# Performance work log

Measured on AMD Instinct MI355X. Metric: run time of the kernel, lower is better.

## Reference

```python
import jax, jax.numpy as jnp
import numpy as np

N = 16384
IN_F = 128
OUT_F = 32


def setup_inputs() -> dict:
    key = jax.random.key(0)
    k1, k2, k3 = jax.random.split(key, 3)
    inp = jax.random.normal(k1, (N, IN_F), dtype=jnp.float32)
    # dense (densified-sparse) adjacency, nonnegative like a normalized adj
    adj = jax.random.uniform(k2, (N, N), dtype=jnp.float32) * (1.0 / N)
    stdv = np.sqrt(1.0 / (IN_F + OUT_F)).astype(np.float32)
    weight = jax.random.uniform(k3, (IN_F, OUT_F), dtype=jnp.float32,
                                minval=-stdv, maxval=stdv)
    return {"input": inp, "adj": adj, "weight": weight}


def reference(input, adj, weight):
    # dropout p=0.0 -> identity (matches nn.Dropout(0.0) / eval mode)
    support = input @ weight          # [N, out_features]
    output = adj @ support            # [N, out_features] neighbor aggregation
    return jax.nn.relu(output)
```

## Files before the change

kernel.cpp:

```cpp
#include <hip/hip_runtime.h>

#define N 16384
#define IN_F 128
#define OUT_F 32
#define NSPLIT 8
#define KR (N / NSPLIT)
#define KC 128
#define CHUNKS (KR / KC)
#define ROWS 32

typedef __attribute__((ext_vector_type(8))) short short8v;
typedef __attribute__((ext_vector_type(4))) float float4v;

#define GLOAD_LDS16(g, l) \
    __builtin_amdgcn_global_load_lds((const __attribute__((address_space(1))) void*)(g), \
                                     (__attribute__((address_space(3))) void*)(l), 16, 0, 0)

__device__ __forceinline__ unsigned short f2bf(float x) {
    unsigned int u = __float_as_uint(x);
    u += 0x7FFFu + ((u >> 16) & 1u);
    return (unsigned short)(u >> 16);
}

__global__ __launch_bounds__(256) void gcn_support(const float* __restrict__ inp,
                                                   const float* __restrict__ w,
                                                   unsigned short* __restrict__ supB) {
    __shared__ float wl[IN_F * OUT_F];
    int tid = threadIdx.x;
#pragma unroll
    for (int u = 0; u < 4; ++u) {
        int idx = (u * 256 + tid) * 4;
        *(float4*)&wl[idx] = *(const float4*)&w[idx];
    }
    __syncthreads();

    int gid = blockIdx.x * 256 + tid;
    int i  = gid >> 2;
    int ks = gid & 3;

    float acc[OUT_F];
#pragma unroll
    for (int j = 0; j < OUT_F; ++j) acc[j] = 0.f;

    const float* ip = inp + (size_t)i * IN_F + ks * 32;
#pragma unroll
    for (int kb = 0; kb < 8; ++kb) {
        float4 a4 = *(const float4*)(ip + kb * 4);
        float av[4] = {a4.x, a4.y, a4.z, a4.w};
#pragma unroll
        for (int kk = 0; kk < 4; ++kk) {
            int k = ks * 32 + kb * 4 + kk;
            const float* wr = &wl[k * OUT_F];
#pragma unroll
            for (int j4 = 0; j4 < 8; ++j4) {
                float4 w4 = *(const float4*)(wr + j4 * 4);
                acc[j4 * 4 + 0] = fmaf(av[kk], w4.x, acc[j4 * 4 + 0]);
                acc[j4 * 4 + 1] = fmaf(av[kk], w4.y, acc[j4 * 4 + 1]);
                acc[j4 * 4 + 2] = fmaf(av[kk], w4.z, acc[j4 * 4 + 2]);
                acc[j4 * 4 + 3] = fmaf(av[kk], w4.w, acc[j4 * 4 + 3]);
            }
        }
    }
#pragma unroll
    for (int j = 0; j < OUT_F; ++j) {
        acc[j] += __shfl_xor(acc[j], 1);
        acc[j] += __shfl_xor(acc[j], 2);
    }
#pragma unroll
    for (int jj = 0; jj < 8; ++jj) {
        int j = ks * 8 + jj;
        supB[(size_t)j * N + i] = f2bf(acc[j]);
    }
}

__global__ __launch_bounds__(256, 5) void gcn_aggregate(const float* __restrict__ adj,
                                                        const unsigned short* __restrict__ supB,
                                                        float* __restrict__ out) {
    __shared__ float sA[2][ROWS * KC];

    int wg = blockIdx.x;
    int rb = wg >> 3;
    int sp = wg & 7;
    int tid  = threadIdx.x;
    int wv   = tid >> 6;
    int lane = tid & 63;
    int mt = wv >> 1;
    int nt = wv & 1;
    int lrow = lane & 15;
    int kgrp = lane >> 4;

    int rowblk = rb * ROWS;
    int kbase  = sp * KR;

    float4v acc = {0.f, 0.f, 0.f, 0.f};

    auto stage = [&](int buf, int c) {
#pragma unroll
        for (int u = 0; u < 4; ++u) {
            int f    = u * 256 + tid;
            int row  = f >> 5;
            int gblk = (f & 31) ^ (row & 7);
            const float* gp = adj + (size_t)(rowblk + row) * N + kbase + c * KC + gblk * 4;
            float* lp = &sA[buf][(u * 256 + wv * 64) * 4];
            GLOAD_LDS16(gp, lp);
        }
    };

    int rowA = mt * 16 + lrow;
    int sw   = rowA & 7;
    const unsigned short* bprow = supB + (size_t)(nt * 16 + lrow) * N + kbase + kgrp * 8;

    stage(0, 0);
    __syncthreads();

    for (int c = 0; c < CHUNKS; ++c) {
        int cur = c & 1;
        if (c + 1 < CHUNKS) stage(cur ^ 1, c + 1);

        const unsigned short* bp = bprow + c * KC;
        short8v b0 = *(const short8v*)(bp + 0);
        short8v b1 = *(const short8v*)(bp + 32);
        short8v b2 = *(const short8v*)(bp + 64);
        short8v b3 = *(const short8v*)(bp + 96);

#pragma unroll
        for (int w = 0; w < 4; ++w) {
            int kw   = w * 32;
            int blk0 = rowA * 32 + (kw >> 2) + kgrp * 2;
            float4 a0 = *(const float4*)&sA[cur][((blk0 ^ sw) << 2)];
            float4 a1 = *(const float4*)&sA[cur][(((blk0 + 1) ^ sw) << 2)];
            short8v af;
            af[0] = (short)f2bf(a0.x); af[1] = (short)f2bf(a0.y);
            af[2] = (short)f2bf(a0.z); af[3] = (short)f2bf(a0.w);
            af[4] = (short)f2bf(a1.x); af[5] = (short)f2bf(a1.y);
            af[6] = (short)f2bf(a1.z); af[7] = (short)f2bf(a1.w);
            short8v bf = (w == 0) ? b0 : (w == 1) ? b1 : (w == 2) ? b2 : b3;
            acc = __builtin_amdgcn_mfma_f32_16x16x32_bf16(af, bf, acc, 0, 0, 0);
        }
        __syncthreads();
    }

    int orow = rowblk + mt * 16 + kgrp * 4;
    int ocol = nt * 16 + lrow;
#pragma unroll
    for (int r = 0; r < 4; ++r)
        atomicAdd(&out[(size_t)(orow + r) * OUT_F + ocol], acc[r]);
}

__global__ __launch_bounds__(256) void gcn_relu(float* __restrict__ out) {
    int gid = blockIdx.x * 256 + threadIdx.x;
    float4* p = (float4*)out;
    float4 v = p[gid];
    v.x = fmaxf(v.x, 0.f);
    v.y = fmaxf(v.y, 0.f);
    v.z = fmaxf(v.z, 0.f);
    v.w = fmaxf(v.w, 0.f);
    p[gid] = v;
}

extern "C" void kernel_launch(void* const* d_in, const int* in_sizes, int n_in,
                              void* d_out, int out_size, void* d_ws, size_t ws_size,
                              hipStream_t stream) {
    (void)in_sizes; (void)n_in; (void)out_size; (void)ws_size;
    const float* inp = (const float*)d_in[0];
    const float* adj = (const float*)d_in[1];
    const float* wgt = (const float*)d_in[2];
    float* out = (float*)d_out;
    unsigned short* supB = (unsigned short*)d_ws;

    hipMemsetAsync(out, 0, (size_t)N * OUT_F * sizeof(float), stream);
    gcn_support<<<(N * 4) / 256, 256, 0, stream>>>(inp, wgt, supB);
    gcn_aggregate<<<(N / ROWS) * NSPLIT, 256, 0, stream>>>(adj, supB, out);
    gcn_relu<<<(N * OUT_F / 4) / 256, 256, 0, stream>>>(out);
}
```

Measured before the change: 251.4 us.

## Replace split-K atomics and LDS staging with in-block split reduction and fused ReLU

The aggregate kernel now gives each block 16 output rows and splits K in two halves across wave pairs. Each wave streams adj straight from global memory into registers, with no LDS double-buffering. The two partial sums are combined through a small shared buffer, and ReLU is applied as the final output is stored. This removes the memset, the global atomicAdds and the separate ReLU launch. In exchange, the two N-tile waves each load the same adj rows, which relies on cache hits, and there is no explicit prefetch pipeline.

```diff
diff --git a/kernel.cpp b/kernel.cpp
--- a/kernel.cpp
+++ b/kernel.cpp
@@ -3,18 +3,11 @@
 #define N 16384
 #define IN_F 128
 #define OUT_F 32
-#define NSPLIT 8
-#define KR (N / NSPLIT)
-#define KC 128
-#define CHUNKS (KR / KC)
-#define ROWS 32
+#define ROWS 16
+#define KH (N / 2)
 
 typedef __attribute__((ext_vector_type(8))) short short8v;
 typedef __attribute__((ext_vector_type(4))) float float4v;
-
-#define GLOAD_LDS16(g, l) \
-    __builtin_amdgcn_global_load_lds((const __attribute__((address_space(1))) void*)(g), \
-                                     (__attribute__((address_space(3))) void*)(l), 16, 0, 0)
 
 __device__ __forceinline__ unsigned short f2bf(float x) {
     unsigned int u = __float_as_uint(x);
@@ -73,89 +66,55 @@
     }
 }
 
-__global__ __launch_bounds__(256, 5) void gcn_aggregate(const float* __restrict__ adj,
+__global__ __launch_bounds__(256, 4) void gcn_aggregate(const float* __restrict__ adj,
                                                         const unsigned short* __restrict__ supB,
                                                         float* __restrict__ out) {
-    __shared__ float sA[2][ROWS * KC];
+    __shared__ float sRed[2][16 * 16];
 
-    int wg = blockIdx.x;
-    int rb = wg >> 3;
-    int sp = wg & 7;
+    int rb   = blockIdx.x;
     int tid  = threadIdx.x;
     int wv   = tid >> 6;
     int lane = tid & 63;
-    int mt = wv >> 1;
     int nt = wv & 1;
-    int lrow = lane & 15;
-    int kgrp = lane >> 4;
+    int kh = wv >> 1;
+    int lr = lane & 15;
+    int kg = lane >> 4;
 
     int rowblk = rb * ROWS;
-    int kbase  = sp * KR;
+    size_t kbase = (size_t)kh * KH + kg * 8;
+
+    const float* ap = adj + (size_t)(rowblk + lr) * N + kbase;
+    const unsigned short* bp = supB + (size_t)(nt * 16 + lr) * N + kbase;
 
     float4v acc = {0.f, 0.f, 0.f, 0.f};
 
-    auto stage = [&](int buf, int c) {
-#pragma unroll
-        for (int u = 0; u < 4; ++u) {
-            int f    = u * 256 + tid;
-            int row  = f >> 5;
-            int gblk = (f & 31) ^ (row & 7);
-            const float* gp = adj + (size_t)(rowblk + row) * N + kbase + c * KC + gblk * 4;
-            float* lp = &sA[buf][(u * 256 + wv * 64) * 4];
-            GLOAD_LDS16(gp, lp);
-        }
-    };
-
-    int rowA = mt * 16 + lrow;
-    int sw   = rowA & 7;
-    const unsigned short* bprow = supB + (size_t)(nt * 16 + lrow) * N + kbase + kgrp * 8;
-
-    stage(0, 0);
-    __syncthreads();
-
-    for (int c = 0; c < CHUNKS; ++c) {
-        int cur = c & 1;
-        if (c + 1 < CHUNKS) stage(cur ^ 1, c + 1);
-
-        const unsigned short* bp = bprow + c * KC;
-        short8v b0 = *(const short8v*)(bp + 0);
-        short8v b1 = *(const short8v*)(bp + 32);
-        short8v b2 = *(const short8v*)(bp + 64);
-        short8v b3 = *(const short8v*)(bp + 96);
-
-#pragma unroll
-        for (int w = 0; w < 4; ++w) {
-            int kw   = w * 32;
-            int blk0 = rowA * 32 + (kw >> 2) + kgrp * 2;
-            float4 a0 = *(const float4*)&sA[cur][((blk0 ^ sw) << 2)];
-            float4 a1 = *(const float4*)&sA[cur][(((blk0 + 1) ^ sw) << 2)];
-            short8v af;
-            af[0] = (short)f2bf(a0.x); af[1] = (short)f2bf(a0.y);
-            af[2] = (short)f2bf(a0.z); af[3] = (short)f2bf(a0.w);
-            af[4] = (short)f2bf(a1.x); af[5] = (short)f2bf(a1.y);
-            af[6] = (short)f2bf(a1.z); af[7] = (short)f2bf(a1.w);
-            short8v bf = (w == 0) ? b0 : (w == 1) ? b1 : (w == 2) ? b2 : b3;
-            acc = __builtin_amdgcn_mfma_f32_16x16x32_bf16(af, bf, acc, 0, 0, 0);
-        }
-        __syncthreads();
+#pragma unroll 4
+    for (int it = 0; it < KH / 32; ++it) {
+        const float* a = ap + (size_t)it * 32;
+        float4 a0 = *(const float4*)(a);
+        float4 a1 = *(const float4*)(a + 4);
+        short8v b = *(const short8v*)(bp + (size_t)it * 32);
+        short8v af;
+        af[0] = (short)f2bf(a0.x); af[1] = (short)f2bf(a0.y);
+        af[2] = (short)f2bf(a0.z); af[3] = (short)f2bf(a0.w);
+        af[4] = (short)f2bf(a1.x); af[5] = (short)f2bf(a1.y);
+        af[6] = (short)f2bf(a1.z); af[7] = (short)f2bf(a1.w);
+        acc = __builtin_amdgcn_mfma_f32_16x16x32_bf16(af, b, acc, 0, 0, 0);
     }
 
-    int orow = rowblk + mt * 16 + kgrp * 4;
-    int ocol = nt * 16 + lrow;
+    if (kh == 1) {
 #pragma unroll
-    for (int r = 0; r < 4; ++r)
-        atomicAdd(&out[(size_t)(orow + r) * OUT_F + ocol], acc[r]);
-}
-
-__global__ __launch_bounds__(256) void gcn_relu(float* __restrict__ out) {
-    int gid = blockIdx.x * 256 + threadIdx.x;
-    float4* p = (float4*)out;
-    float4 v = p[gid];
-    v.x = fmaxf(v.x, 0.f);
-    v.y = fmaxf(v.y, 0.f);
-    v.z = fmaxf(v.z, 0.f);
-    v.w = fmaxf(v.w, 0.f);
-    p[gid] = v;
+        for (int r = 0; r < 4; ++r)
+            sRed[nt][(kg * 4 + r) * 16 + lr] = acc[r];
+    }
+    __syncthreads();
+    if (kh == 0) {
+#pragma unroll
+        for (int r = 0; r < 4; ++r) {
+            float s = acc[r] + sRed[nt][(kg * 4 + r) * 16 + lr];
+            out[(size_t)(rowblk + kg * 4 + r) * OUT_F + nt * 16 + lr] = fmaxf(s, 0.f);
+        }
+    }
 }
 
 extern "C" void kernel_launch(void* const* d_in, const int* in_sizes, int n_in,
@@ -168,8 +127,6 @@
     float* out = (float*)d_out;
     unsigned short* supB = (unsigned short*)d_ws;
 
-    hipMemsetAsync(out, 0, (size_t)N * OUT_F * sizeof(float), stream);
     gcn_support<<<(N * 4) / 256, 256, 0, stream>>>(inp, wgt, supB);
-    gcn_aggregate<<<(N / ROWS) * NSPLIT, 256, 0, stream>>>(adj, supB, out);
-    gcn_relu<<<(N * OUT_F / 4) / 256, 256, 0, stream>>>(out);
+    gcn_aggregate<<<N / ROWS, 256, 0, stream>>>(adj, supB, out);
 }
```

Result: slower. 375.2 us (+49.3%).
